# Kernel tuning notes

Hardware: AMD Instinct MI355X
Metric: run time of the kernel (lower is better)

Reference implementation:

```python
import jax, jax.numpy as jnp
import numpy as np
import math

B, S, D, H = 2, 1024, 1024, 16
HD = D // H          # head dim
KD = 256             # performer kernel dim (LearnedPerformerAttention default)
TOPK = 10            # DynamicSparseAttention k default
NE, NS = 4, 2        # experts, sub-experts


def setup_inputs() -> dict:
    key = jax.random.key(0)
    it = iter(jax.random.split(key, 24))
    def rn(shape, scale=0.02):
        return jax.random.normal(next(it), shape, dtype=jnp.float32) * scale
    z = lambda s: jnp.zeros(s, jnp.float32)
    o = lambda s: jnp.ones(s, jnp.float32)
    return {
        "x": jax.random.normal(next(it), (B, S, D), dtype=jnp.float32),
        "w_qkvo": rn((NE, 4, D, D)), "b_qkvo": z((NE, 4, D)),
        "sp_w": rn((D, 1)), "sp_b": z((1,)),
        "phi_w": rn((HD, KD)), "phi_b": z((KD,)),
        "psi_w": rn((HD, KD)), "psi_b": z((KD,)),
        "conv_dw": rn((3, 1, D)), "conv_pw": rn((D, D)),
        "fus_w": rn((2 * D, D)), "fus_b": z((D,)),
        "sub_w1": rn((NE, NS, D, D)), "sub_b1": z((NE, NS, D)),
        "sub_g": o((NE, NS, D)), "sub_be": z((NE, NS, D)),
        "sub_w2": rn((NE, NS, D, D)), "sub_b2": z((NE, NS, D)),
        "r1_w1": rn((D, D // 2)), "r1_b1": z((D // 2,)),
        "r1_g": o((D // 2,)), "r1_be": z((D // 2,)),
        "r1_w2": rn((D // 2, NE)), "r1_b2": z((NE,)),
        "r2_w1": rn((NE, D, D // 4)), "r2_b1": z((NE, D // 4)),
        "r2_g": o((NE, D // 4)), "r2_be": z((NE, D // 4)),
        "r2_w2": rn((NE, D // 4, NS)), "r2_b2": z((NE, NS)),
    }


def _ln(x, g, b, eps=1e-5):
    mu = x.mean(-1, keepdims=True)
    var = ((x - mu) ** 2).mean(-1, keepdims=True)
    return (x - mu) * jax.lax.rsqrt(var + eps) * g + b


def _heads(t):  # [B,S,D] -> [B,H,S,HD]
    return t.reshape(B, S, H, HD).transpose(0, 2, 1, 3)


def _merge(t):  # [B,H,S,HD] -> [B,S,D]
    return t.transpose(0, 2, 1, 3).reshape(B, S, D)


def _forward(x, w_qkvo, b_qkvo, sp_w, sp_b, phi_w, phi_b, psi_w, psi_b,
             conv_dw, conv_pw, fus_w, fus_b, sub_w1, sub_b1, sub_g, sub_be,
             sub_w2, sub_b2, r1_w1, r1_b1, r1_g, r1_be, r1_w2, r1_b2,
             r2_w1, r2_b1, r2_g, r2_be, r2_w2, r2_b2):
    scale = 1.0 / math.sqrt(HD)

    def proj(i):
        q = _heads(x @ w_qkvo[i, 0] + b_qkvo[i, 0])
        k = _heads(x @ w_qkvo[i, 1] + b_qkvo[i, 1])
        v = _heads(x @ w_qkvo[i, 2] + b_qkvo[i, 2])
        return q, k, v

    def oproj(t, i):
        return t @ w_qkvo[i, 3] + b_qkvo[i, 3]

    # ---- expert 0: DynamicSparseAttention (eval path: learned top-k key mask) ----
    q, k, v = proj(0)
    scores = jnp.einsum('bhqd,bhkd->bhqk', q, k) * scale
    tok_imp = (x @ sp_w + sp_b)[..., 0]                       # [B,S]
    _, top_idx = jax.lax.top_k(tok_imp, TOPK)
    key_mask = jnp.zeros((B, S), x.dtype).at[jnp.arange(B)[:, None], top_idx].set(1.0)
    scores = scores * key_mask[:, None, None, :]
    out0 = oproj(_merge(jax.nn.softmax(scores, axis=-1) @ v), 0)

    # ---- expert 1: LearnedPerformerAttention (linear attention) ----
    q, k, v = proj(1)
    q_phi = jax.nn.elu(q @ phi_w + phi_b) + 1.0               # [B,H,S,KD]
    k_psi = jax.nn.elu(k @ psi_w + psi_b) + 1.0
    kv = jnp.einsum('bhld,bhlm->bhdm', k_psi, v)              # [B,H,KD,HD]
    num = jnp.einsum('bhld,bhdm->bhlm', q_phi, kv)
    den = jnp.einsum('bhld,bhd->bhl', q_phi, k_psi.sum(2))[..., None] + 1e-8
    out1 = oproj(_merge(num / den), 1)

    # ---- expert 2: BaseExpertAttention (standard softmax attention) ----
    q, k, v = proj(2)
    scores = jnp.einsum('bhqd,bhkd->bhqk', q, k) * scale
    out2 = oproj(_merge(jax.nn.softmax(scores, axis=-1) @ v), 2)

    # ---- expert 3: TemporalConvAttention (depthwise temporal conv branch + attn + fusion) ----
    xc = jax.lax.conv_general_dilated(
        x, conv_dw, window_strides=(1,), padding='SAME',
        dimension_numbers=('NWC', 'WIO', 'NWC'), feature_group_count=D)
    xc = jax.nn.gelu(xc @ conv_pw)
    q, k, v = proj(3)
    scores = jnp.einsum('bhqd,bhkd->bhqk', q, k) * scale
    ao = oproj(_merge(jax.nn.softmax(scores, axis=-1) @ v), 3)
    out3 = jnp.concatenate([ao, xc], axis=-1) @ fus_w + fus_b

    expert_outs = [out0, out1, out2, out3]

    # ---- level-1 router ----
    h1 = jax.nn.relu(_ln(x @ r1_w1 + r1_b1, r1_g, r1_be))
    probs_l1 = jax.nn.softmax(h1 @ r1_w2 + r1_b2, axis=-1)    # [B,S,NE]

    final = jnp.zeros_like(x)
    for i, eo in enumerate(expert_outs):
        # level-2 router over sub-experts, conditioned on expert output
        h2 = jax.nn.relu(_ln(eo @ r2_w1[i] + r2_b1[i], r2_g[i], r2_be[i]))
        probs_l2 = jax.nn.softmax(h2 @ r2_w2[i] + r2_b2[i], axis=-1)  # [B,S,NS]
        sub = jnp.zeros_like(eo)
        for j in range(NS):
            s = jax.nn.gelu(_ln(eo @ sub_w1[i, j] + sub_b1[i, j], sub_g[i, j], sub_be[i, j]))
            s = s @ sub_w2[i, j] + sub_b2[i, j]
            sub = sub + probs_l2[..., j:j + 1] * s
        final = final + probs_l1[..., i:i + 1] * sub
    return final


def reference(x, w_qkvo, b_qkvo, sp_w, sp_b, phi_w, phi_b, psi_w, psi_b,
              conv_dw, conv_pw, fus_w, fus_b, sub_w1, sub_b1, sub_g, sub_be,
              sub_w2, sub_b2, r1_w1, r1_b1, r1_g, r1_be, r1_w2, r1_b2,
              r2_w1, r2_b1, r2_g, r2_be, r2_w2, r2_b2):
    return _forward(x, w_qkvo, b_qkvo, sp_w, sp_b, phi_w, phi_b, psi_w, psi_b,
                    conv_dw, conv_pw, fus_w, fus_b, sub_w1, sub_b1, sub_g, sub_be,
                    sub_w2, sub_b2, r1_w1, r1_b1, r1_g, r1_be, r1_w2, r1_b2,
                    r2_w1, r2_b1, r2_g, r2_be, r2_w2, r2_b2)
```

## Files before the change

### kernel.cpp

```cpp
#include <hip/hip_runtime.h>
#include <hip/hip_bf16.h>
#include <cstdint>

using bf16 = __hip_bfloat16;
typedef __attribute__((ext_vector_type(8))) short bfrag;
typedef __attribute__((ext_vector_type(4))) float ffrag;

#define DEV __device__ __forceinline__

DEV float wred_sum(float v) {
#pragma unroll
  for (int o = 32; o > 0; o >>= 1) v += __shfl_xor(v, o, 64);
  return v;
}
DEV float bred_sum(float v) {
  __shared__ float r[4];
  int w = threadIdx.x >> 6, l = threadIdx.x & 63;
  v = wred_sum(v);
  __syncthreads();
  if (l == 0) r[w] = v;
  __syncthreads();
  return r[0] + r[1] + r[2] + r[3];
}
DEV float gelu_f(float x) {
  float x3 = x * x * x;
  return 0.5f * x * (1.0f + tanhf(0.7978845608028654f * (x + 0.044715f * x3)));
}

struct GemmP {
  const bf16* A; const bf16* A2; const bf16* B; void* C; void* C2;
  const float* bias;
  int K, lda, ldb, ldc, inner, mode, zBshift, c2z, kSplit;
  long sA0, sA1, sB0, sB1, sC0, sC1, sb0, sb1;
  float scale;
};
static GemmP gp0() {
  GemmP g;
  g.A = nullptr; g.A2 = nullptr; g.B = nullptr; g.C = nullptr; g.C2 = nullptr;
  g.bias = nullptr;
  g.K = 0; g.lda = 0; g.ldb = 0; g.ldc = 0; g.inner = 1; g.mode = 0;
  g.zBshift = 0; g.c2z = -1; g.kSplit = 1 << 30;
  g.sA0 = 0; g.sA1 = 0; g.sB0 = 0; g.sB1 = 0; g.sC0 = 0; g.sC1 = 0;
  g.sb0 = 0; g.sb1 = 0; g.scale = 1.f;
  return g;
}

template <int BM, int BN, int WM, int WN, bool SPLIT>
__global__ __launch_bounds__(256)
void gemm_nt(GemmP p) {
  constexpr int TI = BM / (WM * 16), TJ = BN / (WN * 16);
  __shared__ bf16 smem[(BM + BN) * 32];
  const int tid = threadIdx.x;
  const int z = blockIdx.z;
  const int z0 = z % p.inner, z1 = z / p.inner;
  const long zB = (long)(z1 >> p.zBshift);
  const bf16* A = p.A + (long)z0 * p.sA0 + (long)z1 * p.sA1;
  const bf16* Bp = p.B + (long)z0 * p.sB0 + zB * p.sB1;
  const int m0 = blockIdx.x * BM, n0 = blockIdx.y * BN;
  const int wave = tid >> 6, lane = tid & 63;
  const int wrow = wave / WN, wcol = wave % WN;
  const int fr = lane & 15, quad = lane >> 4;
  const int swz = (quad ^ ((fr >> 1) & 3)) * 8;
  ffrag acc[TI][TJ] = {};
  constexpr int CH_A = BM * 4;
  constexpr int NIT = (BM + BN) * 4 / 256;
  for (int k0 = 0; k0 < p.K; k0 += 32) {
    const bf16* Asrc = A;
    int kc = k0;
    if constexpr (SPLIT) {
      if (k0 >= p.kSplit) { Asrc = p.A2; kc = k0 - p.kSplit; }
    }
#pragma unroll
    for (int it = 0; it < NIT; ++it) {
      int idx = it * 256 + tid;
      const bf16* g;
      if (idx < CH_A) {
        int r = idx >> 2, c = (idx & 3) ^ ((idx >> 3) & 3);
        g = Asrc + (long)(m0 + r) * p.lda + kc + c * 8;
      } else {
        int j = idx - CH_A;
        int r = j >> 2, c = (j & 3) ^ ((j >> 3) & 3);
        g = Bp + (long)(n0 + r) * p.ldb + k0 + c * 8;
      }
      __builtin_amdgcn_global_load_lds(
          (const __attribute__((address_space(1))) void*)g,
          (__attribute__((address_space(3))) void*)(smem + idx * 8), 16, 0, 0);
    }
    __syncthreads();
    bfrag af[TI], bfb[TJ];
#pragma unroll
    for (int t = 0; t < TI; ++t)
      af[t] = *(const bfrag*)(smem + ((wrow * (TI * 16) + t * 16 + fr) * 32 + swz));
#pragma unroll
    for (int t = 0; t < TJ; ++t)
      bfb[t] = *(const bfrag*)(smem + (BM * 32 + (wcol * (TJ * 16) + t * 16 + fr) * 32 + swz));
#pragma unroll
    for (int ti = 0; ti < TI; ++ti)
#pragma unroll
      for (int tj = 0; tj < TJ; ++tj)
        acc[ti][tj] = __builtin_amdgcn_mfma_f32_16x16x32_bf16(af[ti], bfb[tj], acc[ti][tj], 0, 0, 0);
    __syncthreads();
  }
  const int mbase = m0 + wrow * (TI * 16), nbase = n0 + wcol * (TJ * 16);
  void* Cb = p.C;
  long zc = (long)z0 * p.sC0 + (long)z1 * p.sC1;
  if (z == p.c2z) { Cb = p.C2; zc = 0; }
  const long zb = (long)z0 * p.sb0 + zB * p.sb1;
#pragma unroll
  for (int ti = 0; ti < TI; ++ti) {
#pragma unroll
    for (int tj = 0; tj < TJ; ++tj) {
#pragma unroll
      for (int r = 0; r < 4; ++r) {
        int m = mbase + ti * 16 + quad * 4 + r;
        int n = nbase + tj * 16 + fr;
        float v = acc[ti][tj][r] * p.scale;
        if (p.bias) v += p.bias[zb + n];
        long ci = zc + (long)m * p.ldc + n;
        if (p.mode == 0) ((bf16*)Cb)[ci] = __float2bfloat16(v);
        else if (p.mode == 1) ((float*)Cb)[ci] = v;
        else if (p.mode == 3) ((bf16*)Cb)[ci] = __float2bfloat16(gelu_f(v));
        else if (p.mode == 4) ((bf16*)Cb)[ci] = __float2bfloat16(v > 0.f ? v + 1.f : __expf(v));
        else ((bf16*)Cb)[ci] = __float2bfloat16(__expf(v - 16.f));
      }
    }
  }
}

static void launch_gemm(hipStream_t st, int cfg, int M, int N, int batch, const GemmP& g) {
  dim3 bs(256);
  if (cfg == 0)      gemm_nt<128, 128, 2, 2, false><<<dim3(M / 128, N / 128, batch), bs, 0, st>>>(g);
  else if (cfg == 1) gemm_nt<128, 64, 2, 2, false><<<dim3(M / 128, N / 64, batch), bs, 0, st>>>(g);
  else if (cfg == 2) gemm_nt<64, 64, 2, 2, false><<<dim3(M / 64, N / 64, batch), bs, 0, st>>>(g);
  else               gemm_nt<64, 64, 2, 2, true><<<dim3(M / 64, N / 64, batch), bs, 0, st>>>(g);
}

template <int BM2, int BN2>
__global__ __launch_bounds__(512)
void gemm_nt8(GemmP p) {
  constexpr int TI = BM2 / 32;
  constexpr int TJ = BN2 / 64;
  constexpr int TIP = TI / 4;
  constexpr int BUFEL = (BM2 + BN2) * 64;
  constexpr int NLA = BM2 / 64;
  constexpr int NLB = BN2 / 64;
  __shared__ __align__(16) bf16 smem[2 * BUFEL];
  const int tid = threadIdx.x;

  int bx = blockIdx.x, by = blockIdx.y, z = blockIdx.z;
  {
    const int gX = gridDim.x, gY = gridDim.y;
    const int byzTot = gY * gridDim.z;
    const int nbxg = gX >> 2;
    if (nbxg == 2 || nbxg == 4) {
      const int nbyzg = 8 / nbxg;
      if (byzTot % nbyzg == 0) {
        int lin = bx + gX * (by + gY * z);
        int xcd = lin & 7, q = lin >> 3;
        bx = (xcd % nbxg) * 4 + (q & 3);
        int byz = (xcd / nbxg) * (byzTot / nbyzg) + (q >> 2);
        by = byz % gY; z = byz / gY;
      }
    }
  }

  const int z0 = z % p.inner, z1 = z / p.inner;
  const long zB = (long)(z1 >> p.zBshift);
  const bf16* A = p.A + (long)z0 * p.sA0 + (long)z1 * p.sA1;
  const bf16* Bp = p.B + (long)z0 * p.sB0 + zB * p.sB1;
  const int m0 = bx * BM2, n0 = by * BN2;
  const int wave = tid >> 6, lane = tid & 63;
  const int wrow = wave >> 2, wcol = wave & 3;
  const int fr = lane & 15, quad = lane >> 4;

  const bf16* gsrcA[NLA]; int loffA[NLA];
  const bf16* gsrcB[NLB]; int loffB[NLB];
#pragma unroll
  for (int i = 0; i < NLA; ++i) {
    int idx = i * 512 + tid;
    int r = idx >> 3, cs = idx & 7, c = cs ^ (r & 7);
    gsrcA[i] = A + (long)(m0 + r) * p.lda + c * 8;
    loffA[i] = idx * 8;
  }
#pragma unroll
  for (int j = 0; j < NLB; ++j) {
    int idx = j * 512 + tid;
    int r = idx >> 3, cs = idx & 7, c = cs ^ (r & 7);
    gsrcB[j] = Bp + (long)(n0 + r) * p.ldb + c * 8;
    loffB[j] = BM2 * 64 + idx * 8;
  }
  auto gload = [&](const bf16* g, bf16* l) {
    __builtin_amdgcn_global_load_lds(
        (const __attribute__((address_space(1))) void*)g,
        (__attribute__((address_space(3))) void*)l, 16, 0, 0);
  };

  const int cs0 = (quad ^ (fr & 7)) * 8;
  const int cs1 = ((quad ^ (fr & 7)) ^ 4) * 8;
  const int aBase = (wrow * (BM2 / 2) + fr) * 64;
  const int bBase = BM2 * 64 + (wcol * (TJ * 16) + fr) * 64;

  ffrag acc[TI][TJ] = {};
  const int NT = p.K >> 6;

#pragma unroll
  for (int i = 0; i < NLA; ++i) { gload(gsrcA[i], smem + loffA[i]); gsrcA[i] += 64; }
#pragma unroll
  for (int j = 0; j < NLB; ++j) { gload(gsrcB[j], smem + loffB[j]); gsrcB[j] += 64; }
#pragma unroll
  for (int j = 0; j < NLB; ++j) { gload(gsrcB[j], smem + BUFEL + loffB[j]); gsrcB[j] += 64; }
  asm volatile("s_waitcnt vmcnt(%0)" ::"n"(NLB) : "memory");
  __builtin_amdgcn_s_barrier();
  asm volatile("" ::: "memory");

  for (int kt = 0; kt < NT; ++kt) {
    const int cur = kt & 1;
    const bf16* sb = smem + cur * BUFEL;
    bf16* sCur = smem + cur * BUFEL;
    bf16* sOther = smem + (cur ^ 1) * BUFEL;
    bfrag bb0[TJ], bb1[TJ];
#pragma unroll
    for (int ph = 0; ph < 4; ++ph) {
      if (ph == 0) {
#pragma unroll
        for (int tj = 0; tj < TJ; ++tj) {
          bb0[tj] = *(const bfrag*)(sb + bBase + tj * 1024 + cs0);
          bb1[tj] = *(const bfrag*)(sb + bBase + tj * 1024 + cs1);
        }
      }
      bfrag a0[TIP], a1[TIP];
#pragma unroll
      for (int q = 0; q < TIP; ++q) {
        const int ti = ph * TIP + q;
        a0[q] = *(const bfrag*)(sb + aBase + ti * 1024 + cs0);
        a1[q] = *(const bfrag*)(sb + aBase + ti * 1024 + cs1);
      }
      if (ph < 2) {
        if (kt + 1 < NT) {
#pragma unroll
          for (int i = 0; i < NLA / 2; ++i) {
            const int ii = ph * (NLA / 2) + i;
            gload(gsrcA[ii], sOther + loffA[ii]); gsrcA[ii] += 64;
          }
        }
      } else {
        if (kt + 2 < NT) {
#pragma unroll
          for (int j = 0; j < NLB / 2; ++j) {
            const int jj = (ph - 2) * (NLB / 2) + j;
            gload(gsrcB[jj], sCur + loffB[jj]); gsrcB[jj] += 64;
          }
        }
      }
      if (ph == 3 && kt + 1 < NT) {
        if (kt + 2 < NT) asm volatile("s_waitcnt vmcnt(%0)" ::"n"(NLB) : "memory");
        else             asm volatile("s_waitcnt vmcnt(0)" ::: "memory");
      }
      asm volatile("" ::: "memory");
      __builtin_amdgcn_s_barrier();
      asm volatile("s_waitcnt lgkmcnt(0)" ::: "memory");
      __builtin_amdgcn_sched_barrier(0);
      __builtin_amdgcn_s_setprio(1);
#pragma unroll
      for (int q = 0; q < TIP; ++q) {
        const int ti = ph * TIP + q;
#pragma unroll
        for (int tj = 0; tj < TJ; ++tj) {
          acc[ti][tj] = __builtin_amdgcn_mfma_f32_16x16x32_bf16(a0[q], bb0[tj], acc[ti][tj], 0, 0, 0);
          acc[ti][tj] = __builtin_amdgcn_mfma_f32_16x16x32_bf16(a1[q], bb1[tj], acc[ti][tj], 0, 0, 0);
        }
      }
      __builtin_amdgcn_s_setprio(0);
      asm volatile("" ::: "memory");
      __builtin_amdgcn_s_barrier();
      asm volatile("" ::: "memory");
    }
  }

  const int mbase = m0 + wrow * (BM2 / 2), nbase = n0 + wcol * (TJ * 16);
  void* Cb = p.C;
  long zc = (long)z0 * p.sC0 + (long)z1 * p.sC1;
  if (z == p.c2z) { Cb = p.C2; zc = 0; }
  const long zb = (long)z0 * p.sb0 + zB * p.sb1;
#pragma unroll
  for (int ti = 0; ti < TI; ++ti) {
#pragma unroll
    for (int tj = 0; tj < TJ; ++tj) {
#pragma unroll
      for (int r = 0; r < 4; ++r) {
        int m = mbase + ti * 16 + quad * 4 + r;
        int n = nbase + tj * 16 + fr;
        float v = acc[ti][tj][r] * p.scale;
        if (p.bias) v += p.bias[zb + n];
        ((bf16*)Cb)[zc + (long)m * p.ldc + n] = __float2bfloat16(v);
      }
    }
  }
}

static void launch_gemm8(hipStream_t st, int cfg, int M, int N, int batch, const GemmP& g) {
  if (cfg == 0)
    gemm_nt8<256, 256><<<dim3(M / 256, N / 256, batch), dim3(512), 0, st>>>(g);
  else
    gemm_nt8<128, 256><<<dim3(M / 128, N / 256, batch), dim3(512), 0, st>>>(g);
}

__global__ void prep_k(const float* w_qkvo, const float* sub_w1, const float* sub_w2,
                       const float* conv_pw, const float* fus_w, const float* r1_w1,
                       const float* r2_w1, const float* phi_w, const float* psi_w,
                       const float* phi_b, const float* psi_b,
                       bf16* wt, bf16* fuswt, bf16* r1w1t, bf16* r2w1t,
                       bf16* phiwt, bf16* psiwt, float* phipsib, bf16* vtp1) {
  int z = blockIdx.z;
  int bx = blockIdx.x, by = blockIdx.y;
  int tx = threadIdx.x & 31, ty = threadIdx.x >> 5;
  const float* src; bf16* dst; int R, C;
  if (z < 33) {
    if (by >= 32) return;
    src = z < 16 ? w_qkvo + (long)z * 1048576
        : z < 24 ? sub_w1 + (long)(z - 16) * 1048576
        : z < 32 ? sub_w2 + (long)(z - 24) * 1048576
                 : conv_pw;
    dst = wt + (long)z * 1048576; R = 1024; C = 1024;
  } else if (z == 33) {
    src = fus_w; dst = fuswt; R = 2048; C = 1024;
  } else if (z == 34) {
    if (bx >= 16 || by >= 32) return;
    src = r1_w1; dst = r1w1t; R = 1024; C = 512;
  } else if (z < 39) {
    if (bx >= 8 || by >= 32) return;
    src = r2_w1 + (long)(z - 35) * 262144; dst = r2w1t + (long)(z - 35) * 262144;
    R = 1024; C = 256;
  } else if (z < 41) {
    if (bx >= 8 || by >= 2) return;
    src = (z == 39) ? phi_w : psi_w; dst = (z == 39) ? phiwt : psiwt; R = 64; C = 256;
  } else {
    if (by == 0) {
      for (int c = threadIdx.x; c < 1024; c += 256)
        vtp1[(long)bx * 131072 + 65536 + c] = __float2bfloat16(1.0f);
    } else if (by == 1 && bx == 0) {
      for (int i = threadIdx.x; i < 512; i += 256)
        phipsib[i] = i < 256 ? phi_b[i] : psi_b[i - 256];
    }
    return;
  }
  __shared__ float t[32][33];
  int c0 = bx * 32, r0 = by * 32;
#pragma unroll
  for (int i = 0; i < 32; i += 8)
    t[ty + i][tx] = src[(long)(r0 + ty + i) * C + c0 + tx];
  __syncthreads();
#pragma unroll
  for (int i = 0; i < 32; i += 8)
    dst[(long)(c0 + ty + i) * R + r0 + tx] = __float2bfloat16(t[tx][ty + i]);
}

__global__ void xprep_k(const float* x, const float* dw, const float* spw, const float* spb,
                        bf16* xb, bf16* t1, float* tokimp) {
  long row = blockIdx.x;
  int s = (int)(row & 1023);
  int tid = threadIdx.x;
  const float* xr = x + row * 1024;
  float dot = 0.f;
#pragma unroll
  for (int i = 0; i < 4; ++i) {
    int d = tid + i * 256;
    float xv = xr[d];
    xb[row * 1024 + d] = __float2bfloat16(xv);
    float a = xv * dw[1024 + d];
    if (s > 0) a += xr[d - 1024] * dw[d];
    if (s < 1023) a += xr[d + 1024] * dw[2048 + d];
    t1[row * 1024 + d] = __float2bfloat16(a);
    dot += xv * spw[d];
  }
  float tot = bred_sum(dot);
  if (tid == 0) tokimp[row] = tot + spb[0];
}

__global__ void transpose_bf16_k(const bf16* in, bf16* outp, int R, int C, int rs,
                                 int inner, int inner2, long is0, long is1, long is2,
                                 long ldz) {
  __shared__ bf16 t[32][33];
  int z = blockIdx.z;
  int z0 = z % inner; int zr = z / inner;
  int z1 = zr % inner2; int z2 = zr / inner2;
  long zo = (long)z0 * is0 + (long)z1 * is1 + (long)z2 * is2;
  int c0 = blockIdx.x * 32, r0 = blockIdx.y * 32;
  int tx = threadIdx.x & 31, ty = threadIdx.x >> 5;
#pragma unroll
  for (int i = 0; i < 32; i += 8)
    t[ty + i][tx] = in[zo + (long)(r0 + ty + i) * rs + c0 + tx];
  __syncthreads();
  long ob = (long)z * ldz;
#pragma unroll
  for (int i = 0; i < 32; i += 8)
    outp[ob + (long)(c0 + ty + i) * R + r0 + tx] = t[tx][ty + i];
}

__global__ void vtones_k(bf16* vt) {
  int i = blockIdx.x * 256 + threadIdx.x;
  int z = i >> 10, c = i & 1023;
  vt[(long)z * 131072 + 65536 + c] = __float2bfloat16(1.0f);
}

__global__ void norm_k(const bf16* in, bf16* outp, float eps) {
  int r = blockIdx.x * 4 + (threadIdx.x >> 6);
  int n = threadIdx.x & 63;
  int z = r >> 10, s = r & 1023;
  int h = z & 15, b = z >> 4;
  const bf16* ip = in + (long)r * 128;
  float den = __bfloat162float(ip[64]) + eps;
  float v = __bfloat162float(ip[n]);
  outp[((long)(b * 1024 + s) * 1024) + h * 64 + n] = __float2bfloat16(v / den);
}

__global__ void ln_act_k(const void* in, const float* gamma, const float* beta,
                         bf16* outp, int N, int act, int rows_per_seg, int in_bf16) {
  long row = blockIdx.x;
  int tid = threadIdx.x;
  const bf16* ib = (const bf16*)in;
  const float* iff = (const float*)in;
  float vc[4];
  float ls = 0.f;
  int i = 0;
  for (int c = tid; c < N; c += 256, ++i) {
    float v = in_bf16 ? __bfloat162float(ib[row * N + c]) : iff[row * N + c];
    vc[i] = v; ls += v;
  }
  float mean = bred_sum(ls) / N;
  float lv = 0.f;
  i = 0;
  for (int c = tid; c < N; c += 256, ++i) { float d = vc[i] - mean; lv += d * d; }
  float rstd = rsqrtf(bred_sum(lv) / N + 1e-5f);
  long go = (row / rows_per_seg) * (long)N;
  const float* gp = gamma + go;
  const float* bp = beta + go;
  i = 0;
  for (int c = tid; c < N; c += 256, ++i) {
    float v = (vc[i] - mean) * rstd * gp[c] + bp[c];
    v = act ? gelu_f(v) : fmaxf(v, 0.f);
    outp[row * N + c] = __float2bfloat16(v);
  }
}

__global__ void topk_k(const float* timp, int* outp) {
  __shared__ float vals[1024];
  __shared__ float wv[4];
  __shared__ int wi[4];
  int b = blockIdx.x, tid = threadIdx.x;
  for (int c = tid; c < 1024; c += 256) vals[c] = timp[b * 1024 + c];
  __syncthreads();
  for (int t = 0; t < 10; ++t) {
    float bv = -3.0e38f; int bi = 1 << 30;
    for (int c = tid; c < 1024; c += 256) {
      float v = vals[c];
      if (v > bv || (v == bv && c < bi)) { bv = v; bi = c; }
    }
#pragma unroll
    for (int o = 32; o > 0; o >>= 1) {
      float ov = __shfl_xor(bv, o, 64); int oi = __shfl_xor(bi, o, 64);
      if (ov > bv || (ov == bv && oi < bi)) { bv = ov; bi = oi; }
    }
    int w = tid >> 6, l = tid & 63;
    if (l == 0) { wv[w] = bv; wi[w] = bi; }
    __syncthreads();
    if (tid == 0) {
      float fv = wv[0]; int fi = wi[0];
      for (int ww = 1; ww < 4; ++ww)
        if (wv[ww] > fv || (wv[ww] == fv && wi[ww] < fi)) { fv = wv[ww]; fi = wi[ww]; }
      outp[b * 16 + t] = fi;
      vals[fi] = -3.0e38f;
    }
    __syncthreads();
  }
}

__global__ void vsum_k(const bf16* v, float* vsump) {
  __shared__ float red[4][64];
  int zz = blockIdx.x;
  int z = zz >> 4, slab = zz & 15;
  int b = z >> 4, h = z & 15;
  const bf16* vp = v + (long)b * 1048576 + h * 64;
  int d = threadIdx.x & 63, sg = threadIdx.x >> 6;
  float s = 0.f;
#pragma unroll
  for (int i = 0; i < 16; ++i) {
    int srow = slab * 64 + sg * 16 + i;
    s += __bfloat162float(vp[(long)srow * 1024 + d]);
  }
  red[sg][d] = s;
  __syncthreads();
  if (sg == 0) vsump[(long)zz * 64 + d] = red[0][d] + red[1][d] + red[2][d] + red[3][d];
}

__global__ void sparse_attn_k(const bf16* q, const bf16* k, const bf16* v,
                              const float* vsump, const int* topidx, bf16* merged) {
  __shared__ float kt[10][64], vt[10][64], vs[64], vts[64];
  int z = blockIdx.y, b = z >> 4, h = z & 15;
  int tid = threadIdx.x;
  const int* tix = topidx + b * 16;
  for (int t = tid; t < 640; t += 256) {
    int tt = t >> 6, d = t & 63;
    long src = ((long)b * 1024 + tix[tt]) * 1024 + h * 64 + d;
    kt[tt][d] = __bfloat162float(k[src]);
    vt[tt][d] = __bfloat162float(v[src]);
  }
  if (tid < 64) {
    float s = 0.f;
#pragma unroll
    for (int p = 0; p < 16; ++p) s += vsump[((long)z * 16 + p) * 64 + tid];
    vs[tid] = s;
  }
  __syncthreads();
  if (tid < 64) {
    float s = 0.f;
#pragma unroll
    for (int t = 0; t < 10; ++t) s += vt[t][tid];
    vts[tid] = s;
  }
  __syncthreads();
  int wave = tid >> 6, lane = tid & 63;
  int sq = blockIdx.x * 4 + wave;
  long qi = ((long)b * 1024 + sq) * 1024 + h * 64 + lane;
  float qd = __bfloat162float(q[qi]);
  float sc[10];
#pragma unroll
  for (int t = 0; t < 10; ++t) sc[t] = wred_sum(qd * kt[t][lane]) * 0.125f;
  float m = 0.f;
#pragma unroll
  for (int t = 0; t < 10; ++t) m = fmaxf(m, sc[t]);
  float e[10], se = 0.f;
#pragma unroll
  for (int t = 0; t < 10; ++t) { e[t] = __expf(sc[t] - m); se += e[t]; }
  float em = __expf(-m);
  float Z = 1014.f * em + se;
  float o = em * (vs[lane] - vts[lane]);
#pragma unroll
  for (int t = 0; t < 10; ++t) o += e[t] * vt[t][lane];
  merged[qi] = __float2bfloat16(o / Z);
}

__global__ void router1_k(const bf16* h1, const float* w, const float* bias, float* outp) {
  int row = blockIdx.x * 4 + (threadIdx.x >> 6);
  int l = threadIdx.x & 63;
  const bf16* hp = h1 + (long)row * 512;
  float a0 = 0, a1 = 0, a2 = 0, a3 = 0;
  for (int c = l; c < 512; c += 64) {
    float hv = __bfloat162float(hp[c]);
    const float* wp = w + c * 4;
    a0 += hv * wp[0]; a1 += hv * wp[1]; a2 += hv * wp[2]; a3 += hv * wp[3];
  }
  a0 = wred_sum(a0); a1 = wred_sum(a1); a2 = wred_sum(a2); a3 = wred_sum(a3);
  a0 += bias[0]; a1 += bias[1]; a2 += bias[2]; a3 += bias[3];
  float m = fmaxf(fmaxf(a0, a1), fmaxf(a2, a3));
  float e0 = __expf(a0 - m), e1 = __expf(a1 - m), e2 = __expf(a2 - m), e3 = __expf(a3 - m);
  float inv = 1.f / (e0 + e1 + e2 + e3);
  if (l == 0) {
    float* op = outp + (long)row * 4;
    op[0] = e0 * inv; op[1] = e1 * inv; op[2] = e2 * inv; op[3] = e3 * inv;
  }
}

__global__ void router2_k(const bf16* h2, const float* w, const float* bias, float* outp,
                          int rows_per_seg) {
  int row = blockIdx.x * 4 + (threadIdx.x >> 6);
  int l = threadIdx.x & 63;
  int seg = row / rows_per_seg;
  const float* wp = w + (long)seg * 512;
  const float* bp = bias + (long)seg * 2;
  const bf16* hp = h2 + (long)row * 256;
  float a0 = 0, a1 = 0;
  for (int c = l; c < 256; c += 64) {
    float hv = __bfloat162float(hp[c]);
    a0 += hv * wp[c * 2]; a1 += hv * wp[c * 2 + 1];
  }
  a0 = wred_sum(a0); a1 = wred_sum(a1);
  a0 += bp[0]; a1 += bp[1];
  float m = fmaxf(a0, a1);
  float e0 = __expf(a0 - m), e1 = __expf(a1 - m);
  float inv = 1.f / (e0 + e1);
  if (l == 0) { outp[(long)row * 2] = e0 * inv; outp[(long)row * 2 + 1] = e1 * inv; }
}

__global__ void combine_k(const bf16* part, const float* p1, const float* p2, float* outp) {
  long i = (long)blockIdx.x * 256 + threadIdx.x;
  long m = i >> 10;
  float acc = 0.f;
#pragma unroll
  for (int zz = 0; zz < 8; ++zz) {
    int e = zz >> 1, j = zz & 1;
    float w = p1[m * 4 + e] * p2[(long)e * 4096 + m * 2 + j];
    acc += w * __bfloat162float(part[(long)zz * 2097152 + i]);
  }
  outp[i] = acc;
}

extern "C" void kernel_launch(void* const* d_in, const int* in_sizes, int n_in,
                              void* d_out, int out_size, void* d_ws, size_t ws_size,
                              hipStream_t stream) {
  const float* x = (const float*)d_in[0];
  const float* w_qkvo = (const float*)d_in[1];
  const float* b_qkvo = (const float*)d_in[2];
  const float* sp_w = (const float*)d_in[3];
  const float* sp_b = (const float*)d_in[4];
  const float* phi_w = (const float*)d_in[5];
  const float* phi_b = (const float*)d_in[6];
  const float* psi_w = (const float*)d_in[7];
  const float* psi_b = (const float*)d_in[8];
  const float* conv_dw = (const float*)d_in[9];
  const float* conv_pw = (const float*)d_in[10];
  const float* fus_w = (const float*)d_in[11];
  const float* fus_b = (const float*)d_in[12];
  const float* sub_w1 = (const float*)d_in[13];
  const float* sub_b1 = (const float*)d_in[14];
  const float* sub_g = (const float*)d_in[15];
  const float* sub_be = (const float*)d_in[16];
  const float* sub_w2 = (const float*)d_in[17];
  const float* sub_b2 = (const float*)d_in[18];
  const float* r1_w1 = (const float*)d_in[19];
  const float* r1_b1 = (const float*)d_in[20];
  const float* r1_g = (const float*)d_in[21];
  const float* r1_be = (const float*)d_in[22];
  const float* r1_w2 = (const float*)d_in[23];
  const float* r1_b2 = (const float*)d_in[24];
  const float* r2_w1 = (const float*)d_in[25];
  const float* r2_b1 = (const float*)d_in[26];
  const float* r2_g = (const float*)d_in[27];
  const float* r2_be = (const float*)d_in[28];
  const float* r2_w2 = (const float*)d_in[29];
  const float* r2_b2 = (const float*)d_in[30];
  (void)in_sizes; (void)n_in; (void)ws_size; (void)out_size;

  char* ws = (char*)d_ws;
  size_t off = 0;
  auto take = [&](size_t bytes) { void* p = ws + off; off += (bytes + 255) & ~(size_t)255; return p; };

  const long EL2M = 2097152;
  const long EL1M = 1048576;

  bf16* XB      = (bf16*)take((size_t)EL2M * 2);
  bf16* WQKVOT  = (bf16*)take((size_t)16 * EL1M * 2);
  bf16* SUBW1T  = (bf16*)take((size_t)8 * EL1M * 2);
  bf16* SUBW2T  = (bf16*)take((size_t)8 * EL1M * 2);
  bf16* CONVPWT = (bf16*)take((size_t)EL1M * 2);
  bf16* FUSWT   = (bf16*)take((size_t)EL2M * 2);
  bf16* R1W1T   = (bf16*)take((size_t)512 * 1024 * 2);
  bf16* R2W1T   = (bf16*)take((size_t)4 * 256 * 1024 * 2);
  bf16* PHIWT   = (bf16*)take((size_t)16384 * 2);
  bf16* PSIWT   = (bf16*)take((size_t)16384 * 2);
  float* PHIPSIB = (float*)take((size_t)512 * 4);
  bf16* QKVB    = (bf16*)take((size_t)12 * EL2M * 2);
  bf16* MERGED4 = (bf16*)take((size_t)4 * EL2M * 2);
  bf16* VTP1    = (bf16*)take((size_t)32 * 128 * 1024 * 2);
  bf16* EO      = (bf16*)take((size_t)4 * EL2M * 2);
  bf16* T1      = (bf16*)take((size_t)EL2M * 2);
  bf16* ARENA   = (bf16*)take((size_t)64 * 1024 * 1024);
  float* PROBS1 = (float*)take((size_t)2048 * 4 * 4);
  float* PROBS2 = (float*)take((size_t)4 * 2048 * 2 * 4);
  float* TOKIMP = (float*)take((size_t)2048 * 4);
  int*   TOPIDX = (int*)take((size_t)2 * 16 * 4);
  float* VSUMP  = (float*)take((size_t)32 * 16 * 64 * 4);

  bf16* QPHI  = ARENA;
  bf16* KPSI  = ARENA + 8388608;
  bf16* KPSIT = ARENA + 16777216;
  bf16* KVTX  = ARENA + 25165824;
  bf16* SC = ARENA;
  bf16* SUB2F = ARENA;
  float* F32TMP = (float*)(ARENA + 16777216);
  bf16* H1 = ARENA + 20971520;
  bf16* H2 = ARENA + 22020096;
  bf16* AO = ARENA + 24117248;
  bf16* XC = ARENA + 26214400;
  bf16* TNUM23 = QKVB;
  bf16* VT23   = QKVB + 2 * EL2M;
  bf16* SUB1A = QKVB;
  bf16* SUB1B = QKVB + 16777216;

  prep_k<<<dim3(32, 64, 42), 256, 0, stream>>>(w_qkvo, sub_w1, sub_w2, conv_pw, fus_w,
                                               r1_w1, r2_w1, phi_w, psi_w, phi_b, psi_b,
                                               WQKVOT, FUSWT, R1W1T, R2W1T,
                                               PHIWT, PSIWT, PHIPSIB, VTP1);
  xprep_k<<<2048, 256, 0, stream>>>(x, conv_dw, sp_w, sp_b, XB, T1, TOKIMP);

  {
    GemmP g = gp0();
    g.A = XB; g.lda = 1024;
    g.B = WQKVOT; g.ldb = 1024; g.sB0 = EL1M; g.sB1 = 4 * EL1M;
    g.C = QKVB; g.ldc = 1024; g.sC0 = EL2M; g.sC1 = 3 * EL2M;
    g.bias = b_qkvo; g.sb0 = 1024; g.sb1 = 4096;
    g.K = 1024; g.inner = 3; g.mode = 0;
    launch_gemm8(stream, 1, 2048, 1024, 12, g);
  }

  topk_k<<<2, 256, 0, stream>>>(TOKIMP, TOPIDX);
  vsum_k<<<512, 256, 0, stream>>>(QKVB + 2 * EL2M, VSUMP);
  sparse_attn_k<<<dim3(256, 32), 256, 0, stream>>>(QKVB, QKVB + EL2M, QKVB + 2 * EL2M,
                                                   VSUMP, TOPIDX, MERGED4);

  {
    GemmP g = gp0();
    g.A = QKVB + 3 * EL2M; g.lda = 1024; g.sA0 = 64; g.sA1 = EL1M;
    g.B = PHIWT; g.ldb = 64; g.sB1 = 16384; g.zBshift = 1;
    g.C = QPHI; g.ldc = 256; g.sC0 = 262144; g.sC1 = 16 * 262144L;
    g.bias = PHIPSIB; g.sb1 = 256;
    g.K = 64; g.inner = 16; g.mode = 4;
    launch_gemm(stream, 2, 1024, 256, 64, g);
  }
  transpose_bf16_k<<<dim3(8, 32, 32), 256, 0, stream>>>(KPSI, KPSIT, 1024, 256, 256,
                                                        32, 1, 262144, 0, 0, 262144);
  transpose_bf16_k<<<dim3(2, 32, 32), 256, 0, stream>>>(QKVB + 5 * EL2M, VTP1, 1024, 64, 1024,
                                                        16, 2, 64, EL1M, 0, 131072);
  {
    GemmP g = gp0();
    g.A = VTP1; g.lda = 1024; g.sA0 = 131072; g.sA1 = 16 * 131072L;
    g.B = KPSIT; g.ldb = 1024; g.sB0 = 262144; g.sB1 = 16 * 262144L;
    g.C = KVTX; g.ldc = 256; g.sC0 = 32768; g.sC1 = 16 * 32768L;
    g.K = 1024; g.inner = 16; g.mode = 0;
    launch_gemm(stream, 2, 128, 256, 32, g);
  }
  {
    GemmP g = gp0();
    g.A = QPHI; g.lda = 256; g.sA0 = 262144; g.sA1 = 16 * 262144L;
    g.B = KVTX; g.ldb = 256; g.sB0 = 32768; g.sB1 = 16 * 32768L;
    g.C = VTP1; g.ldc = 128; g.sC0 = 131072; g.sC1 = 16 * 131072L;
    g.K = 256; g.inner = 16; g.mode = 0;
    launch_gemm(stream, 2, 1024, 128, 32, g);
  }
  norm_k<<<8192, 256, 0, stream>>>(VTP1, MERGED4 + EL2M, 1e-8f);

  transpose_bf16_k<<<dim3(2, 32, 64), 256, 0, stream>>>(QKVB + 8 * EL2M, VT23, 1024, 64, 1024,
                                                        16, 2, 64, EL1M, 3 * EL2M, 131072);
  vtones_k<<<256, 256, 0, stream>>>(VT23);

  for (int e = 2; e <= 3; ++e) {
    const bf16* q = QKVB + (size_t)(e * 3 + 0) * EL2M;
    const bf16* k = QKVB + (size_t)(e * 3 + 1) * EL2M;
    {
      GemmP g = gp0();
      g.A = q; g.lda = 1024; g.sA0 = 64; g.sA1 = EL1M;
      g.B = k; g.ldb = 1024; g.sB0 = 64; g.sB1 = EL1M;
      g.C = SC; g.ldc = 1024; g.sC0 = EL1M; g.sC1 = 16 * EL1M;
      g.K = 64; g.inner = 16; g.scale = 0.125f; g.mode = 6;
      launch_gemm(stream, 0, 1024, 1024, 32, g);
    }
    {
      GemmP g = gp0();
      g.A = SC; g.lda = 1024; g.sA0 = EL1M; g.sA1 = 16 * EL1M;
      g.B = VT23 + (size_t)(e - 2) * 32 * 131072; g.ldb = 1024; g.sB0 = 131072; g.sB1 = 16 * 131072L;
      g.C = TNUM23; g.ldc = 128; g.sC0 = 131072; g.sC1 = 16 * 131072L;
      g.K = 1024; g.inner = 16; g.mode = 0;
      launch_gemm(stream, 2, 1024, 128, 32, g);
    }
    norm_k<<<8192, 256, 0, stream>>>(TNUM23, MERGED4 + (size_t)e * EL2M, 0.f);
  }

  {
    GemmP g = gp0();
    g.A = MERGED4; g.lda = 1024; g.sA1 = EL2M;
    g.B = WQKVOT + 3 * EL1M; g.ldb = 1024; g.sB1 = 4 * EL1M;
    g.C = EO; g.ldc = 1024; g.sC1 = EL2M;
    g.C2 = AO; g.c2z = 3;
    g.bias = b_qkvo + 3 * 1024; g.sb1 = 4096;
    g.K = 1024; g.mode = 0;
    launch_gemm8(stream, 1, 2048, 1024, 4, g);
  }

  {
    GemmP g = gp0();
    g.A = T1; g.lda = 1024;
    g.B = CONVPWT; g.ldb = 1024;
    g.C = XC; g.ldc = 1024;
    g.K = 1024; g.mode = 3;
    launch_gemm(stream, 2, 2048, 1024, 1, g);
  }
  {
    GemmP g = gp0();
    g.A = AO; g.A2 = XC; g.kSplit = 1024; g.lda = 1024;
    g.B = FUSWT; g.ldb = 2048;
    g.C = EO + 3 * EL2M; g.ldc = 1024;
    g.bias = fus_b; g.K = 2048; g.mode = 0;
    launch_gemm(stream, 3, 2048, 1024, 1, g);
  }

  {
    GemmP g = gp0();
    g.A = XB; g.lda = 1024;
    g.B = R1W1T; g.ldb = 1024;
    g.C = F32TMP; g.ldc = 512;
    g.bias = r1_b1; g.K = 1024; g.mode = 1;
    launch_gemm(stream, 2, 2048, 512, 1, g);
  }
  ln_act_k<<<2048, 256, 0, stream>>>(F32TMP, r1_g, r1_be, H1, 512, 0, 2048, 0);
  router1_k<<<512, 256, 0, stream>>>(H1, r1_w2, r1_b2, PROBS1);
  {
    GemmP g = gp0();
    g.A = EO; g.lda = 1024; g.sA1 = EL2M;
    g.B = R2W1T; g.ldb = 1024; g.sB1 = 262144;
    g.C = F32TMP; g.ldc = 256; g.sC1 = 2048 * 256;
    g.bias = r2_b1; g.sb1 = 256; g.K = 1024; g.mode = 1;
    launch_gemm(stream, 2, 2048, 256, 4, g);
  }
  ln_act_k<<<8192, 256, 0, stream>>>(F32TMP, r2_g, r2_be, H2, 256, 0, 2048, 0);
  router2_k<<<2048, 256, 0, stream>>>(H2, r2_w2, r2_b2, PROBS2, 2048);

  {
    GemmP g = gp0();
    g.A = EO; g.lda = 1024; g.sA1 = EL2M;
    g.B = SUBW1T; g.ldb = 1024; g.sB0 = EL1M; g.sB1 = 2 * EL1M;
    g.C = SUB1A; g.ldc = 1024; g.sC0 = EL2M; g.sC1 = 2 * EL2M;
    g.bias = sub_b1; g.sb0 = 1024; g.sb1 = 2048;
    g.K = 1024; g.inner = 2; g.mode = 0;
    launch_gemm8(stream, 0, 2048, 1024, 8, g);
  }
  ln_act_k<<<16384, 256, 0, stream>>>(SUB1A, sub_g, sub_be, SUB1B, 1024, 1, 2048, 1);
  {
    GemmP g = gp0();
    g.A = SUB1B; g.lda = 1024; g.sA1 = EL2M;
    g.B = SUBW2T; g.ldb = 1024; g.sB1 = EL1M;
    g.C = SUB2F; g.ldc = 1024; g.sC1 = EL2M;
    g.bias = sub_b2; g.sb1 = 1024;
    g.K = 1024; g.mode = 0;
    launch_gemm8(stream, 0, 2048, 1024, 8, g);
  }
  combine_k<<<8192, 256, 0, stream>>>(SUB2F, PROBS1, PROBS2, (float*)d_out);
}
```

Before: 899.7 us.

## Fuse softmax-attention score, exp and PV GEMMs into one flash-style kernel

After: 792.5 us. -11.9%, faster.

```diff
diff --git a/kernel.cpp b/kernel.cpp
--- a/kernel.cpp
+++ b/kernel.cpp
@@ -25,6 +25,13 @@
 DEV float gelu_f(float x) {
   float x3 = x * x * x;
   return 0.5f * x * (1.0f + tanhf(0.7978845608028654f * (x + 0.044715f * x3)));
+}
+DEV uint32_t pack2bf(float lo, float hi) {
+  bf16 a = __float2bfloat16(lo), b = __float2bfloat16(hi);
+  unsigned short ua, ub;
+  __builtin_memcpy(&ua, &a, 2);
+  __builtin_memcpy(&ub, &b, 2);
+  return (uint32_t)ua | ((uint32_t)ub << 16);
 }
 
 struct GemmP {
@@ -303,6 +310,141 @@
     gemm_nt8<256, 256><<<dim3(M / 256, N / 256, batch), dim3(512), 0, st>>>(g);
   else
     gemm_nt8<128, 256><<<dim3(M / 128, N / 256, batch), dim3(512), 0, st>>>(g);
+}
+
+__global__ __launch_bounds__(256)
+void fused_attn_k(const bf16* qkvb, const bf16* vt23, bf16* out2, bf16* out3) {
+  __shared__ __align__(16) bf16 Ks[2][64 * 64];
+  __shared__ __align__(16) bf16 Vs[2][96 * 64];
+  __shared__ __align__(16) bf16 Ps[4][32 * 64];
+  const int tid = threadIdx.x;
+  const int wave = tid >> 6, lane = tid & 63;
+  const int fr = lane & 15, quad = lane >> 4;
+  const int zz = blockIdx.y, z = zz & 31;
+  const int e = 2 + (zz >> 5);
+  const int h = z & 15, b = z >> 4;
+  const long base = (long)b * 1048576 + h * 64;
+  const bf16* qb = qkvb + (long)(e * 3 + 0) * 2097152 + base;
+  const bf16* kb0 = qkvb + (long)(e * 3 + 1) * 2097152 + base;
+  const bf16* vtb = vt23 + ((long)(e - 2) * 32 + z) * 131072;
+  bf16* outp = (e == 2 ? out2 : out3) + (long)z * 131072;
+  const int m0 = blockIdx.x * 128;
+
+  bfrag qf[2][2];
+#pragma unroll
+  for (int nf = 0; nf < 2; ++nf)
+#pragma unroll
+    for (int dk = 0; dk < 2; ++dk)
+      qf[nf][dk] = *(const bfrag*)(qb + (long)(m0 + wave * 32 + nf * 16 + fr) * 1024 + dk * 32 + quad * 8);
+
+  const bf16* gK[2]; int lK[2];
+#pragma unroll
+  for (int i = 0; i < 2; ++i) {
+    int idx = i * 256 + tid;
+    int r = idx >> 3, c = (idx & 7) ^ (r & 7);
+    gK[i] = kb0 + (long)r * 1024 + c * 8;
+    lK[i] = idx * 8;
+  }
+  const bf16* gV[3]; int lV[3];
+#pragma unroll
+  for (int i = 0; i < 3; ++i) {
+    int idx = i * 256 + tid;
+    int r = idx >> 3, c = (idx & 7) ^ (r & 7);
+    gV[i] = vtb + (long)r * 1024 + c * 8;
+    lV[i] = idx * 8;
+  }
+  auto stage = [&](int buf) {
+#pragma unroll
+    for (int i = 0; i < 2; ++i) {
+      __builtin_amdgcn_global_load_lds(
+          (const __attribute__((address_space(1))) void*)gK[i],
+          (__attribute__((address_space(3))) void*)(Ks[buf] + lK[i]), 16, 0, 0);
+      gK[i] += 64 * 1024;
+    }
+#pragma unroll
+    for (int i = 0; i < 3; ++i) {
+      __builtin_amdgcn_global_load_lds(
+          (const __attribute__((address_space(1))) void*)gV[i],
+          (__attribute__((address_space(3))) void*)(Vs[buf] + lV[i]), 16, 0, 0);
+      gV[i] += 64;
+    }
+  };
+  stage(0);
+  stage(1);
+
+  const int cs0 = (quad ^ (fr & 7)) * 8;
+  const int cs1 = ((quad ^ 4) ^ (fr & 7)) * 8;
+  bf16* myP = Ps[wave];
+  ffrag av[5][2] = {};
+
+  for (int kt = 0; kt < 16; ++kt) {
+    const int cur = kt & 1;
+    if (kt < 15) asm volatile("s_waitcnt vmcnt(5)" ::: "memory");
+    else         asm volatile("s_waitcnt vmcnt(0)" ::: "memory");
+    __builtin_amdgcn_s_barrier();
+    asm volatile("" ::: "memory");
+    const bf16* kbuf = Ks[cur];
+    const bf16* vbuf = Vs[cur];
+
+    ffrag s[4][2] = {};
+#pragma unroll
+    for (int kf = 0; kf < 4; ++kf) {
+      bfrag ka0 = *(const bfrag*)(kbuf + (kf * 16 + fr) * 64 + cs0);
+      bfrag ka1 = *(const bfrag*)(kbuf + (kf * 16 + fr) * 64 + cs1);
+#pragma unroll
+      for (int nf = 0; nf < 2; ++nf) {
+        s[kf][nf] = __builtin_amdgcn_mfma_f32_16x16x32_bf16(ka0, qf[nf][0], s[kf][nf], 0, 0, 0);
+        s[kf][nf] = __builtin_amdgcn_mfma_f32_16x16x32_bf16(ka1, qf[nf][1], s[kf][nf], 0, 0, 0);
+      }
+    }
+#pragma unroll
+    for (int kf = 0; kf < 4; ++kf)
+#pragma unroll
+      for (int nf = 0; nf < 2; ++nf) {
+        float e0 = __expf(s[kf][nf][0] * 0.125f - 16.f);
+        float e1 = __expf(s[kf][nf][1] * 0.125f - 16.f);
+        float e2 = __expf(s[kf][nf][2] * 0.125f - 16.f);
+        float e3 = __expf(s[kf][nf][3] * 0.125f - 16.f);
+        int c2 = (kf * 2 + (quad >> 1)) ^ (fr & 7);
+        uint2 w; w.x = pack2bf(e0, e1); w.y = pack2bf(e2, e3);
+        *(uint2*)(myP + (nf * 16 + fr) * 64 + c2 * 8 + (quad & 1) * 4) = w;
+      }
+    asm volatile("" ::: "memory");
+    asm volatile("s_waitcnt lgkmcnt(0)" ::: "memory");
+    __builtin_amdgcn_sched_barrier(0);
+#pragma unroll
+    for (int ks = 0; ks < 2; ++ks) {
+      const int pcs = ks ? cs1 : cs0;
+      bfrag pb[2];
+#pragma unroll
+      for (int nf = 0; nf < 2; ++nf)
+        pb[nf] = *(const bfrag*)(myP + (nf * 16 + fr) * 64 + pcs);
+#pragma unroll
+      for (int ti = 0; ti < 5; ++ti) {
+        bfrag va = *(const bfrag*)(vbuf + (ti * 16 + fr) * 64 + pcs);
+#pragma unroll
+        for (int nf = 0; nf < 2; ++nf)
+          av[ti][nf] = __builtin_amdgcn_mfma_f32_16x16x32_bf16(va, pb[nf], av[ti][nf], 0, 0, 0);
+      }
+    }
+    asm volatile("" ::: "memory");
+    __builtin_amdgcn_s_barrier();
+    asm volatile("" ::: "memory");
+    if (kt < 14) stage(cur);
+  }
+
+#pragma unroll
+  for (int nf = 0; nf < 2; ++nf) {
+    bf16* orow = outp + (long)(m0 + wave * 32 + nf * 16 + fr) * 128;
+#pragma unroll
+    for (int ti = 0; ti < 4; ++ti) {
+      uint2 w;
+      w.x = pack2bf(av[ti][nf][0], av[ti][nf][1]);
+      w.y = pack2bf(av[ti][nf][2], av[ti][nf][3]);
+      *(uint2*)(orow + ti * 16 + quad * 4) = w;
+    }
+    if (quad == 0) orow[64] = __float2bfloat16(av[4][nf][0]);
+  }
 }
 
 __global__ void prep_k(const float* w_qkvo, const float* sub_w1, const float* sub_w2,
@@ -397,10 +539,12 @@
     outp[ob + (long)(c0 + ty + i) * R + r0 + tx] = t[tx][ty + i];
 }
 
-__global__ void vtones_k(bf16* vt) {
-  int i = blockIdx.x * 256 + threadIdx.x;
-  int z = i >> 10, c = i & 1023;
-  vt[(long)z * 131072 + 65536 + c] = __float2bfloat16(1.0f);
+__global__ void vtinit_k(bf16* vt) {
+  long i = (long)blockIdx.x * 256 + threadIdx.x;
+  int slice = (int)(i >> 15);
+  int row = 64 + (int)((i >> 10) & 31);
+  int col = (int)(i & 1023);
+  vt[(long)slice * 131072 + (long)row * 1024 + col] = __float2bfloat16(row == 64 ? 1.0f : 0.0f);
 }
 
 __global__ void norm_k(const bf16* in, bf16* outp, float eps) {
@@ -665,7 +809,6 @@
   bf16* KPSI  = ARENA + 8388608;
   bf16* KPSIT = ARENA + 16777216;
   bf16* KVTX  = ARENA + 25165824;
-  bf16* SC = ARENA;
   bf16* SUB2F = ARENA;
   float* F32TMP = (float*)(ARENA + 16777216);
   bf16* H1 = ARENA + 20971520;
@@ -731,29 +874,11 @@
 
   transpose_bf16_k<<<dim3(2, 32, 64), 256, 0, stream>>>(QKVB + 8 * EL2M, VT23, 1024, 64, 1024,
                                                         16, 2, 64, EL1M, 3 * EL2M, 131072);
-  vtones_k<<<256, 256, 0, stream>>>(VT23);
-
-  for (int e = 2; e <= 3; ++e) {
-    const bf16* q = QKVB + (size_t)(e * 3 + 0) * EL2M;
-    const bf16* k = QKVB + (size_t)(e * 3 + 1) * EL2M;
-    {
-      GemmP g = gp0();
-      g.A = q; g.lda = 1024; g.sA0 = 64; g.sA1 = EL1M;
-      g.B = k; g.ldb = 1024; g.sB0 = 64; g.sB1 = EL1M;
-      g.C = SC; g.ldc = 1024; g.sC0 = EL1M; g.sC1 = 16 * EL1M;
-      g.K = 64; g.inner = 16; g.scale = 0.125f; g.mode = 6;
-      launch_gemm(stream, 0, 1024, 1024, 32, g);
-    }
-    {
-      GemmP g = gp0();
-      g.A = SC; g.lda = 1024; g.sA0 = EL1M; g.sA1 = 16 * EL1M;
-      g.B = VT23 + (size_t)(e - 2) * 32 * 131072; g.ldb = 1024; g.sB0 = 131072; g.sB1 = 16 * 131072L;
-      g.C = TNUM23; g.ldc = 128; g.sC0 = 131072; g.sC1 = 16 * 131072L;
-      g.K = 1024; g.inner = 16; g.mode = 0;
-      launch_gemm(stream, 2, 1024, 128, 32, g);
-    }
-    norm_k<<<8192, 256, 0, stream>>>(TNUM23, MERGED4 + (size_t)e * EL2M, 0.f);
-  }
+  vtinit_k<<<8192, 256, 0, stream>>>(VT23);
+
+  fused_attn_k<<<dim3(8, 64), 256, 0, stream>>>(QKVB, VT23, TNUM23, VTP1);
+  norm_k<<<8192, 256, 0, stream>>>(TNUM23, MERGED4 + 2 * EL2M, 0.f);
+  norm_k<<<8192, 256, 0, stream>>>(VTP1, MERGED4 + 3 * EL2M, 0.f);
 
   {
     GemmP g = gp0();
```
